# Performance work log

Hardware: AMD Instinct MI355X
Metric: run time of the kernel (lower is better)

The kernel has to match this reference:

```python
import jax, jax.numpy as jnp
import numpy as np
from jax import lax

OUT_SIZE = 224  # original input spatial size (output_size of anomaly map)
NUM_NEIGHBORS = 9
SIGMA = 4.0
KSIZE = 2 * int(4.0 * SIGMA + 0.5) + 1  # 33, kornia-style kernel size


def avg_pool3(x):
    # AvgPool2d(3, 1, 1), count_include_pad=True -> sum over 3x3 window / 9
    s = lax.reduce_window(x, 0.0, lax.add, (1, 1, 3, 3), (1, 1, 1, 1),
                          [(0, 0), (0, 0), (1, 1), (1, 1)])
    return s / 9.0


def euclidean_dist(x, y):
    # x: [..., N, E], y: [..., M, E] -> [..., N, M]
    x_norm = jnp.sum(x * x, axis=-1, keepdims=True)
    y_norm = jnp.sum(y * y, axis=-1, keepdims=True)
    res = x_norm - 2.0 * jnp.matmul(x, jnp.swapaxes(y, -2, -1)) + jnp.swapaxes(y_norm, -2, -1)
    return jnp.sqrt(jnp.clip(res, 0.0))


def gaussian_blur(x):
    # x: [B,1,H,W]; separable Gaussian, reflect padding (kornia GaussianBlur2d default)
    r = KSIZE // 2
    t = jnp.arange(KSIZE, dtype=x.dtype) - r
    k = jnp.exp(-(t * t) / (2.0 * SIGMA * SIGMA))
    k = k / jnp.sum(k)
    xp = jnp.pad(x, ((0, 0), (0, 0), (r, r), (r, r)), mode='reflect')
    kh = k.reshape(1, 1, KSIZE, 1)
    kw = k.reshape(1, 1, 1, KSIZE)
    y = lax.conv_general_dilated(xp, kh, (1, 1), 'VALID',
                                 dimension_numbers=('NCHW', 'OIHW', 'NCHW'))
    return lax.conv_general_dilated(y, kw, (1, 1), 'VALID',
                                    dimension_numbers=('NCHW', 'OIHW', 'NCHW'))


def compute_anomaly_score(patch_scores, locations, embedding, memory_bank):
    # patch_scores/locations: [B, P]; embedding: [B*P, E]; memory_bank: [M, E]
    batch, num_patches = patch_scores.shape
    bidx = jnp.arange(batch)
    max_patches = jnp.argmax(patch_scores, axis=1)                       # [B]
    max_feats = embedding.reshape(batch, num_patches, -1)[bidx, max_patches]  # [B,E]
    score = patch_scores[bidx, max_patches]                              # [B]
    nn_index = locations[bidx, max_patches]                              # [B]
    nn_sample = memory_bank[nn_index]                                    # [B,E]
    n_nb = min(NUM_NEIGHBORS, memory_bank.shape[0])
    d_bank = euclidean_dist(nn_sample, memory_bank)                      # [B,M]
    _, support = lax.top_k(-d_bank, n_nb)                                # [B,k] smallest
    sup_feats = memory_bank[support]                                     # [B,k,E]
    d = euclidean_dist(max_feats[:, None, :], sup_feats)[:, 0, :]        # [B,k]
    weights = (1.0 - jax.nn.softmax(d, axis=1))[:, 0]                    # [B]
    return weights * score


def setup_inputs() -> dict:
    key = jax.random.key(0)
    k1, k2, k3 = jax.random.split(key, 3)
    feat2 = jax.random.normal(k1, (8, 512, 28, 28), dtype=jnp.float32)
    feat3 = jax.random.normal(k2, (8, 1024, 14, 14), dtype=jnp.float32)
    memory_bank = jax.random.normal(k3, (20000, 1536), dtype=jnp.float32)
    return {'feat2': feat2, 'feat3': feat3, 'memory_bank': memory_bank}


def reference(feat2, feat3, memory_bank):
    # feature pooling (AvgPool2d(3,1,1) on each backbone layer)
    f2 = avg_pool3(feat2)
    f3 = avg_pool3(feat3)
    batch, _, height, width = f2.shape
    # generate_embedding: bilinear upsample deeper layer, concat along channels
    f3u = jax.image.resize(f3, (batch, f3.shape[1], height, width), method='bilinear')
    emb = jnp.concatenate([f2, f3u], axis=1)                 # [B,1536,28,28]
    emb_dim = emb.shape[1]
    embedding = emb.transpose(0, 2, 3, 1).reshape(-1, emb_dim)  # [B*784, 1536]
    # nearest_neighbors with n_neighbors=1
    dist = euclidean_dist(embedding, memory_bank)            # [N, M]
    patch_scores = jnp.min(dist, axis=1)
    locations = jnp.argmin(dist, axis=1)
    patch_scores = patch_scores.reshape(batch, -1)
    locations = locations.reshape(batch, -1)
    pred_score = compute_anomaly_score(patch_scores, locations, embedding, memory_bank)
    # anomaly map: bilinear upsample patch scores to input size + gaussian blur
    score_map = patch_scores.reshape(batch, 1, width, height)
    amap = jax.image.resize(score_map, (batch, 1, OUT_SIZE, OUT_SIZE), method='bilinear')
    anomaly_map = gaussian_blur(amap)
    return anomaly_map, pred_score
```

## Files before the change

### kernel.cpp

```cpp
#include <hip/hip_runtime.h>
#include <math.h>

#define NB 8
#define C2 512
#define C3 1024
#define H2 28
#define W2 28
#define H3 14
#define W3 14
#define EDIM 1536
#define PPB (H2*W2)
#define NPATCH (NB*PPB)
#define MPAD 6400
#define MBANK 20000
#define NBPAD 20096
#define NBG (NBPAD/16)
#define OUTW 224
#define NNB 9
#define KS 33
#define KR 16
#define NMT 25
#define NNTB 157
#define CHUNKS 8
#define CH (MBANK/CHUNKS)
#define MPB 64
#define NSLAB 24
#define GRPB (NSLAB*1024)

#define SXQ 63.5f
#define SYQ (127.0f/6.0f)

typedef __attribute__((ext_vector_type(4))) int   i32x4;

#define LEXLT(va,ia,vb,ib) ((va) < (vb) || ((va)==(vb) && (ia)<(ib)))
#define CSWAP(va,ia,vb,ib) { if (LEXLT(va,ia,vb,ib)) { float _tv=(vb); int _ti=(ib); (vb)=(va); (ib)=(ia); (va)=_tv; (ia)=_ti; } }

#define BAR() asm volatile("s_barrier" ::: "memory")

__device__ __forceinline__ signed char q8(float x, float s) {
  int v = (int)rintf(x * s);
  v = v > 127 ? 127 : (v < -127 ? -127 : v);
  return (signed char)v;
}
__device__ __forceinline__ size_t pk_addr(int row, int c) {
  return ((size_t)((row >> 4)*NSLAB + (c >> 6)) << 10)
       + (((c >> 4) & 3) << 8) + ((row & 15) << 4) + (c & 15);
}


__global__ __launch_bounds__(256) void pool2_kernel(const float* __restrict__ in,
    float* __restrict__ emb32, signed char* __restrict__ embp) {
  int bid = blockIdx.x;
  int cg = bid & 7; int h = (bid >> 3) % H2; int b = bid / (8*H2);
  int t = threadIdx.x;
  __shared__ float s3[3][64][29];
  for (int li = t; li < 3*64*28; li += 256) {
    int w = li % 28; int c = (li/28) & 63; int dh = li/(28*64);
    int hh = h + dh - 1;
    float v = 0.f;
    if (hh >= 0 && hh < H2) v = in[((size_t)(b*C2) + cg*64 + c)*784 + hh*28 + w];
    s3[dh][c][w] = v;
  }
  __syncthreads();
  for (int o = t; o < 64*28; o += 256) {
    int c = o & 63, w = o >> 6;
    float s = 0.f;
    #pragma unroll
    for (int dh = 0; dh < 3; ++dh) {
      s += s3[dh][c][w];
      if (w > 0)  s += s3[dh][c][w-1];
      if (w < 27) s += s3[dh][c][w+1];
    }
    s *= (1.f/9.f);
    int row = b*PPB + h*28 + w;
    int cc = cg*64 + c;
    emb32[(size_t)row*EDIM + cc] = s;
    embp[pk_addr(row, cc)] = q8(s, SXQ);
  }
}

__global__ void pool3_kernel(const float* __restrict__ in, float* __restrict__ f3p) {
  int id = blockIdx.x*blockDim.x + threadIdx.x;
  if (id >= NB*C3*H3*W3) return;
  int w = id % W3, h = (id / W3) % H3, c = (id / (H3*W3)) % C3, b = id / (C3*H3*W3);
  const float* src = in + (size_t)(b*C3 + c)*H3*W3;
  float s = 0.f;
  #pragma unroll
  for (int dh=-1; dh<=1; ++dh) {
    int hh = h+dh; if (hh<0||hh>=H3) continue;
    #pragma unroll
    for (int dw=-1; dw<=1; ++dw) {
      int ww = w+dw; if (ww<0||ww>=W3) continue;
      s += src[hh*W3+ww];
    }
  }
  f3p[(size_t)id] = s * (1.f/9.f);
}

__global__ __launch_bounds__(256) void up3_kernel(const float* __restrict__ f3p,
    float* __restrict__ emb32, signed char* __restrict__ embp) {
  int bid = blockIdx.x;
  int cg = bid & 15; int i = (bid >> 4) % H2; int b = bid / (16*H2);
  int t = threadIdx.x;
  float sy = i*0.5f - 0.25f; sy = fminf(fmaxf(sy,0.f),(float)(H3-1));
  int y0 = (int)sy; int y1 = min(y0+1,H3-1); float fy = sy - (float)y0;
  __shared__ float r2[2][64][15];
  for (int li = t; li < 2*64*14; li += 256) {
    int w = li % 14; int c = (li/14) & 63; int yy = li/(14*64);
    int ysrc = yy ? y1 : y0;
    r2[yy][c][w] = f3p[((size_t)(b*C3) + cg*64 + c)*196 + ysrc*14 + w];
  }
  __syncthreads();
  for (int o = t; o < 64*28; o += 256) {
    int c = o & 63, j = o >> 6;
    float sx = j*0.5f - 0.25f; sx = fminf(fmaxf(sx,0.f),(float)(W3-1));
    int x0 = (int)sx; int x1 = min(x0+1,W3-1); float fx = sx - (float)x0;
    float v = (1.f-fy)*((1.f-fx)*r2[0][c][x0] + fx*r2[0][c][x1])
            +      fy *((1.f-fx)*r2[1][c][x0] + fx*r2[1][c][x1]);
    int row = b*PPB + i*28 + j;
    int cc = C2 + cg*64 + c;
    emb32[(size_t)row*EDIM + cc] = v;
    embp[pk_addr(row, cc)] = q8(v, SXQ);
  }
}


__global__ void bank_yn_kernel(const float* __restrict__ bank, float* __restrict__ yn) {
  int w = (blockIdx.x*blockDim.x + threadIdx.x) >> 6;
  int lane = threadIdx.x & 63;
  if (w >= MBANK) return;
  const float4* p = reinterpret_cast<const float4*>(bank + (size_t)w*EDIM);
  float acc = 0.f;
  #pragma unroll
  for (int k = 0; k < EDIM/4/64; ++k) {
    float4 v = p[lane + k*64];
    acc = fmaf(v.x,v.x,acc); acc = fmaf(v.y,v.y,acc);
    acc = fmaf(v.z,v.z,acc); acc = fmaf(v.w,v.w,acc);
  }
  #pragma unroll
  for (int s = 32; s; s >>= 1) acc += __shfl_xor(acc, s);
  if (lane == 0) yn[w] = acc;
}

__global__ __launch_bounds__(256) void bank_pack_kernel(const float* __restrict__ bank,
                                                        signed char* __restrict__ bankp) {
  int grp = blockIdx.x;
  int t = threadIdx.x;
  #pragma unroll
  for (int q = 0; q < 6; ++q) {
    int chunk = t + 256*q;
    int p = chunk >> 6, l = chunk & 63;
    int h = l & 15, gg = l >> 4;
    int row = grp*16 + h;
    int o16[4] = {0,0,0,0};
    if (row < MBANK) {
      const float* src = bank + (size_t)row*EDIM + p*64 + gg*16;
      signed char* oc = (signed char*)o16;
      #pragma unroll
      for (int e = 0; e < 16; ++e) oc[e] = q8(src[e], SYQ);
    }
    *reinterpret_cast<int4*>(bankp + (size_t)grp*GRPB + (size_t)chunk*16) =
        make_int4(o16[0], o16[1], o16[2], o16[3]);
  }
}


__global__ __launch_bounds__(512, 4) void dist_min_i8(
    const signed char* __restrict__ Apk, const signed char* __restrict__ Bpk,
    const float* __restrict__ yn, float* __restrict__ outq, int* __restrict__ outi)
{
  __shared__ __align__(16) unsigned char LDSC[4096];
  const int t = threadIdx.x;
  const int lane = t & 63, wid = t >> 6;
  const int wr = wid >> 1, wc = wid & 1;

  const int nwg = NMT*NNTB;
  int orig = blockIdx.x;
  int xcd = orig & 7, loc = orig >> 3;
  int qq = nwg >> 3, rm = nwg & 7;
  int wg = (xcd < rm ? xcd*(qq+1) : rm*(qq+1) + (xcd-rm)*qq) + loc;
  const int mt = wg / NNTB, nt = wg % NNTB;
  const int m0 = mt*256, n0 = nt*128;

  const signed char* ap[4];
  const signed char* bp[4];
  #pragma unroll
  for (int i = 0; i < 4; ++i) {
    int m16 = (m0 >> 4) + wr*4 + i;
    ap[i] = Apk + (size_t)m16*GRPB + lane*16;
  }
  #pragma unroll
  for (int j = 0; j < 4; ++j) {
    int n16 = (n0 >> 4) + wc*4 + j;
    bp[j] = Bpk + (size_t)n16*GRPB + lane*16;
  }

  i32x4 acc[4][4];
  #pragma unroll
  for (int i = 0; i < 4; ++i)
    #pragma unroll
    for (int j = 0; j < 4; ++j) acc[i][j] = (i32x4){0,0,0,0};

  #pragma unroll 2
  for (int p = 0; p < NSLAB; ++p) {
    i32x4 af[4], bfv[4];
    #pragma unroll
    for (int j = 0; j < 4; ++j)
      bfv[j] = *(const i32x4*)(bp[j] + (size_t)p*1024);
    #pragma unroll
    for (int i = 0; i < 4; ++i)
      af[i] = *(const i32x4*)(ap[i] + (size_t)p*1024);
    __builtin_amdgcn_s_setprio(1);
    #pragma unroll
    for (int i = 0; i < 4; ++i)
      #pragma unroll
      for (int j = 0; j < 4; ++j)
        acc[i][j] = __builtin_amdgcn_mfma_i32_16x16x64_i8(af[i], bfv[j], acc[i][j], 0, 0, 0);
    __builtin_amdgcn_s_setprio(0);
    BAR();
  }

  const float NEG2INV = -2.0f * (2.0f/127.0f) * (6.0f/127.0f);
  const int h = lane & 15, g = lane >> 4;
  float ynv[4];
  #pragma unroll
  for (int j = 0; j < 4; ++j) {
    int col = n0 + wc*64 + j*16 + h;
    ynv[j] = col < MBANK ? yn[col] : INFINITY;
  }
  float* smin = (float*)LDSC;
  int* sidx = (int*)(LDSC + 2048);
  #pragma unroll
  for (int i = 0; i < 4; ++i) {
    #pragma unroll
    for (int r = 0; r < 4; ++r) {
      float v = INFINITY; int ix = 0x7fffffff;
      #pragma unroll
      for (int j = 0; j < 4; ++j) {
        float q = fmaf(NEG2INV, (float)acc[i][j][r], ynv[j]);
        int col = n0 + wc*64 + j*16 + h;
        if (q < v || (q == v && col < ix)) { v = q; ix = col; }
      }
      #pragma unroll
      for (int m = 1; m < 16; m <<= 1) {
        float ov = __shfl_xor(v, m);
        int   oi = __shfl_xor(ix, m);
        if (ov < v || (ov == v && oi < ix)) { v = ov; ix = oi; }
      }
      if (h == 0) {
        int rl = wr*64 + i*16 + g*4 + r;
        smin[rl*2 + wc] = v;
        sidx[rl*2 + wc] = ix;
      }
    }
  }
  __syncthreads();
  if (t < 256) {
    float v0 = smin[t*2], v1 = smin[t*2+1];
    int   i0 = sidx[t*2], i1 = sidx[t*2+1];
    float v; int ix;
    if (LEXLT(v1, i1, v0, i0)) { v = v1; ix = i1; } else { v = v0; ix = i0; }
    int row = m0 + t;
    if (row < NPATCH) {
      outq[(size_t)nt*NPATCH + row] = v;
      outi[(size_t)nt*NPATCH + row] = ix;
    }
  }
}


__global__ __launch_bounds__(256) void minrescore_kernel(
    const float* __restrict__ outq, const int* __restrict__ outi,
    const float* __restrict__ emb32, const float* __restrict__ bank,
    const float* __restrict__ yn, int* __restrict__ loc, float* __restrict__ ps) {
  int w = (blockIdx.x*blockDim.x + threadIdx.x) >> 6;
  int lane = threadIdx.x & 63;
  if (w >= NPATCH) return;
  float bv = INFINITY; int bi = 0x7fffffff;
  for (int s = lane; s < NNTB; s += 64) {
    float v = outq[(size_t)s*NPATCH + w];
    int  ix = outi[(size_t)s*NPATCH + w];
    if (LEXLT(v, ix, bv, bi)) { bv = v; bi = ix; }
  }
  #pragma unroll
  for (int m = 32; m; m >>= 1) {
    float ov = __shfl_xor(bv, m);
    int   oi = __shfl_xor(bi, m);
    if (LEXLT(ov, oi, bv, bi)) { bv = ov; bi = oi; }
  }
  int j = bi;
  if (lane == 0) loc[w] = j;
  const float4* x = reinterpret_cast<const float4*>(emb32 + (size_t)w*EDIM);
  const float4* y = reinterpret_cast<const float4*>(bank + (size_t)j*EDIM);
  float accd = 0.f, accx = 0.f;
  #pragma unroll
  for (int k = 0; k < EDIM/4/64; ++k) {
    float4 a = x[lane + k*64], b = y[lane + k*64];
    accd = fmaf(a.x,b.x,accd); accd = fmaf(a.y,b.y,accd);
    accd = fmaf(a.z,b.z,accd); accd = fmaf(a.w,b.w,accd);
    accx = fmaf(a.x,a.x,accx); accx = fmaf(a.y,a.y,accx);
    accx = fmaf(a.z,a.z,accx); accx = fmaf(a.w,a.w,accx);
  }
  #pragma unroll
  for (int s = 32; s; s >>= 1) { accd += __shfl_xor(accd, s); accx += __shfl_xor(accx, s); }
  if (lane == 0) ps[w] = sqrtf(fmaxf(accx - 2.f*accd + yn[j], 0.f));
}


__global__ void argmax_kernel(const float* __restrict__ ps, const int* __restrict__ loc,
                              float* __restrict__ bscore, int* __restrict__ brow, int* __restrict__ bnn) {
  __shared__ float sv[256]; __shared__ int si[256];
  int b = blockIdx.x, t = threadIdx.x;
  float bv = -INFINITY; int bi = 0x7fffffff;
  for (int p = t; p < PPB; p += 256) {
    float v = ps[b*PPB + p];
    if (v > bv || (v == bv && p < bi)) { bv = v; bi = p; }
  }
  sv[t] = bv; si[t] = bi; __syncthreads();
  for (int s = 128; s; s >>= 1) {
    if (t < s) {
      if (sv[t+s] > sv[t] || (sv[t+s] == sv[t] && si[t+s] < si[t])) { sv[t] = sv[t+s]; si[t] = si[t+s]; }
    }
    __syncthreads();
  }
  if (t == 0) {
    bscore[b] = sv[0];
    brow[b]   = b*PPB + si[0];
    bnn[b]    = loc[b*PPB + si[0]];
  }
}

__global__ __launch_bounds__(256) void dbank_kernel(
    const float* __restrict__ bank, const float* __restrict__ yn,
    const int* __restrict__ bnn, float* __restrict__ dbank)
{
  __shared__ float xs[8][EDIM];
  int t = threadIdx.x;
  for (int idx = t*4; idx < 8*EDIM; idx += 256*4) {
    int b = idx / EDIM, k = idx % EDIM;
    float4 v = *reinterpret_cast<const float4*>(bank + (size_t)bnn[b]*EDIM + k);
    *reinterpret_cast<float4*>(&xs[b][k]) = v;
  }
  __syncthreads();
  int lane = t & 63, w = t >> 6;
  for (int u = 0; u < MPB/4; ++u) {
    int m = blockIdx.x*MPB + u*4 + w;
    if (m < MBANK) {
      const float4* yp = reinterpret_cast<const float4*>(bank + (size_t)m*EDIM);
      float acc[8] = {0.f,0.f,0.f,0.f,0.f,0.f,0.f,0.f};
      for (int k4 = lane; k4 < EDIM/4; k4 += 64) {
        float4 y = yp[k4];
        int k = k4*4;
        #pragma unroll
        for (int b = 0; b < 8; ++b) {
          acc[b] = fmaf(y.x, xs[b][k+0], acc[b]);
          acc[b] = fmaf(y.y, xs[b][k+1], acc[b]);
          acc[b] = fmaf(y.z, xs[b][k+2], acc[b]);
          acc[b] = fmaf(y.w, xs[b][k+3], acc[b]);
        }
      }
      #pragma unroll
      for (int b = 0; b < 8; ++b) {
        float a = acc[b];
        #pragma unroll
        for (int s = 32; s; s >>= 1) a += __shfl_xor(a, s);
        acc[b] = a;
      }
      if (lane == 0) {
        #pragma unroll
        for (int b = 0; b < 8; ++b) {
          int nn = bnn[b];
          float d2 = yn[nn] - 2.f*acc[b] + yn[m];
          dbank[(size_t)b*MBANK + m] = sqrtf(fmaxf(d2, 0.f));
        }
      }
    }
  }
}


__global__ __launch_bounds__(256) void top9_stage1(const float* __restrict__ dbank,
                                                   float* __restrict__ cv, int* __restrict__ ci) {
  int b = blockIdx.x / CHUNKS, ch = blockIdx.x % CHUNKS;
  const float* db = dbank + (size_t)b*MBANK + ch*CH;
  int t = threadIdx.x;

  float v0=INFINITY,v1=INFINITY,v2=INFINITY,v3=INFINITY,v4=INFINITY,
        v5=INFINITY,v6=INFINITY,v7=INFINITY,v8=INFINITY;
  int i0=0x7fffffff,i1=0x7fffffff,i2=0x7fffffff,i3=0x7fffffff,i4=0x7fffffff,
      i5=0x7fffffff,i6=0x7fffffff,i7=0x7fffffff,i8=0x7fffffff;

  for (int s = 0; s < (CH+255)/256; ++s) {
    int m = t + s*256;
    if (m < CH) {
      float nv = db[m]; int ni = ch*CH + m;
      if (LEXLT(nv,ni,v8,i8)) {
        v8 = nv; i8 = ni;
        CSWAP(v8,i8,v7,i7); CSWAP(v7,i7,v6,i6); CSWAP(v6,i6,v5,i5); CSWAP(v5,i5,v4,i4);
        CSWAP(v4,i4,v3,i3); CSWAP(v3,i3,v2,i2); CSWAP(v2,i2,v1,i1); CSWAP(v1,i1,v0,i0);
      }
    }
  }

  __shared__ float sv[256*9];
  __shared__ int   si[256*9];
  __shared__ float rv[256]; __shared__ int ri[256]; __shared__ int rp[256];
  sv[t*9+0]=v0; sv[t*9+1]=v1; sv[t*9+2]=v2; sv[t*9+3]=v3; sv[t*9+4]=v4;
  sv[t*9+5]=v5; sv[t*9+6]=v6; sv[t*9+7]=v7; sv[t*9+8]=v8;
  si[t*9+0]=i0; si[t*9+1]=i1; si[t*9+2]=i2; si[t*9+3]=i3; si[t*9+4]=i4;
  si[t*9+5]=i5; si[t*9+6]=i6; si[t*9+7]=i7; si[t*9+8]=i8;
  __syncthreads();

  for (int r = 0; r < NNB; ++r) {
    float bv = INFINITY; int bix = 0x7fffffff; int bp = -1;
    #pragma unroll
    for (int u = 0; u < 9; ++u) {
      float v = sv[t*9+u]; int ix = si[t*9+u];
      if (LEXLT(v,ix,bv,bix)) { bv = v; bix = ix; bp = t*9+u; }
    }
    rv[t] = bv; ri[t] = bix; rp[t] = bp; __syncthreads();
    for (int s = 128; s; s >>= 1) {
      if (t < s) {
        if (LEXLT(rv[t+s],ri[t+s],rv[t],ri[t])) { rv[t]=rv[t+s]; ri[t]=ri[t+s]; rp[t]=rp[t+s]; }
      }
      __syncthreads();
    }
    if (t == 0) {
      cv[blockIdx.x*NNB + r] = rv[0];
      ci[blockIdx.x*NNB + r] = ri[0];
      sv[rp[0]] = INFINITY; si[rp[0]] = 0x7fffffff;
    }
    __syncthreads();
  }
}


__global__ __launch_bounds__(128) void finalize_kernel(
    const float* __restrict__ cv, const int* __restrict__ ci,
    const float* __restrict__ emb32, const float* __restrict__ bank,
    const float* __restrict__ yn, const int* __restrict__ brow,
    const float* __restrict__ bscore, float* __restrict__ out) {
  __shared__ float sv[128]; __shared__ int si[128];
  __shared__ float wv[128]; __shared__ int wi[128]; __shared__ int wp[128];
  __shared__ int supp[NNB]; __shared__ float ds[NNB];
  int b = blockIdx.x, t = threadIdx.x;
  if (t < CHUNKS*NNB) { sv[t] = cv[b*CHUNKS*NNB + t]; si[t] = ci[b*CHUNKS*NNB + t]; }
  else { sv[t] = INFINITY; si[t] = 0x7fffffff; }
  __syncthreads();
  for (int r = 0; r < NNB; ++r) {
    wv[t] = sv[t]; wi[t] = si[t]; wp[t] = t; __syncthreads();
    for (int s = 64; s; s >>= 1) {
      if (t < s) {
        if (LEXLT(wv[t+s],wi[t+s],wv[t],wi[t])) { wv[t]=wv[t+s]; wi[t]=wi[t+s]; wp[t]=wp[t+s]; }
      }
      __syncthreads();
    }
    if (t == 0) {
      supp[r] = wi[0];
      sv[wp[0]] = INFINITY; si[wp[0]] = 0x7fffffff;
    }
    __syncthreads();
  }
  int lane = t & 63, w = t >> 6;
  int row = brow[b];
  const float* x = emb32 + (size_t)row*EDIM;
  for (int j = w; j < NNB; j += 2) {
    const float* y = bank + (size_t)supp[j]*EDIM;
    float accd = 0.f, accx = 0.f;
    for (int k = lane; k < EDIM; k += 64) {
      float a = x[k];
      accd = fmaf(a, y[k], accd);
      accx = fmaf(a, a, accx);
    }
    #pragma unroll
    for (int s = 32; s; s >>= 1) { accd += __shfl_xor(accd, s); accx += __shfl_xor(accx, s); }
    if (lane == 0) ds[j] = sqrtf(fmaxf(accx - 2.f*accd + yn[supp[j]], 0.f));
  }
  __syncthreads();
  if (t == 0) {
    float mx = -INFINITY;
    #pragma unroll
    for (int j = 0; j < NNB; ++j) mx = fmaxf(mx, ds[j]);
    float s = 0.f;
    #pragma unroll
    for (int j = 0; j < NNB; ++j) s += expf(ds[j] - mx);
    float wgt = 1.f - expf(ds[0] - mx) / s;
    out[b] = wgt * bscore[b];
  }
}


__device__ __forceinline__ int refl224(int x) {
  if (x < 0) return -x;
  if (x > OUTW-1) return 2*(OUTW-1) - x;
  return x;
}

__global__ __launch_bounds__(256) void upblurh_kernel(const float* __restrict__ ps,
                                                      float* __restrict__ tmp) {
  int b = blockIdx.x / OUTW, i = blockIdx.x % OUTW;
  int t = threadIdx.x;
  __shared__ float l[W2];
  __shared__ float graw[KS];
  if (t < KS) {
    float x = (float)t - (float)KR;
    graw[t] = expf(-(x*x) / (2.f*4.f*4.f));
  }
  float sy = ((float)i + 0.5f)*0.125f - 0.5f; sy = fminf(fmaxf(sy,0.f),(float)(H2-1));
  int y0 = (int)sy; int y1 = min(y0+1,H2-1); float fy = sy - (float)y0;
  if (t < W2) {
    const float* p = ps + b*PPB;
    l[t] = (1.f-fy)*p[y0*W2+t] + fy*p[y1*W2+t];
  }
  __syncthreads();
  if (t >= OUTW) return;
  float gsum = 0.f;
  #pragma unroll
  for (int u = 0; u < KS; ++u) gsum += graw[u];
  float winv = 1.f / gsum;
  float s = 0.f;
  #pragma unroll
  for (int v = 0; v < KS; ++v) {
    int jj = refl224(t - KR + v);
    float sx = ((float)jj + 0.5f)*0.125f - 0.5f; sx = fminf(fmaxf(sx,0.f),(float)(W2-1));
    int x0 = (int)sx; int x1 = min(x0+1,W2-1); float fx = sx - (float)x0;
    s = fmaf(graw[v]*winv, (1.f-fx)*l[x0] + fx*l[x1], s);
  }
  tmp[((size_t)b*OUTW + i)*OUTW + t] = s;
}

__global__ __launch_bounds__(256) void blurv_kernel(const float* __restrict__ in,
                                                    float* __restrict__ out) {
  __shared__ float graw[KS];
  int t = threadIdx.x;
  if (t < KS) {
    float x = (float)t - (float)KR;
    graw[t] = expf(-(x*x) / (2.f*4.f*4.f));
  }
  __syncthreads();
  int id = blockIdx.x*blockDim.x + t;
  if (id >= NB*OUTW*OUTW) return;
  float gsum = 0.f;
  #pragma unroll
  for (int u = 0; u < KS; ++u) gsum += graw[u];
  float winv = 1.f / gsum;
  int j = id % OUTW, i = (id/OUTW) % OUTW, b = id/(OUTW*OUTW);
  float s = 0.f;
  #pragma unroll
  for (int u = 0; u < KS; ++u) {
    int ii = refl224(i - KR + u);
    s = fmaf(graw[u]*winv, in[((size_t)b*OUTW + ii)*OUTW + j], s);
  }
  out[id] = s;
}


extern "C" void kernel_launch(void* const* d_in, const int* in_sizes, int n_in,
                              void* d_out, int out_size, void* d_ws, size_t ws_size,
                              hipStream_t stream) {
  const float* feat2 = (const float*)d_in[0];
  const float* feat3 = (const float*)d_in[1];
  const float* bank  = (const float*)d_in[2];
  float* out = (float*)d_out;

  char* base = (char*)d_ws;
  size_t off = 0;
  auto alloc = [&](size_t nbytes) -> char* {
    char* p = base + off;
    off += ((nbytes + 255) & ~(size_t)255);
    return p;
  };
  float*       emb32 = (float*)      alloc((size_t)NPATCH*EDIM*4);
  signed char* embp  = (signed char*)alloc((size_t)(MPAD/16)*GRPB);
  signed char* bankp = (signed char*)alloc((size_t)NBG*GRPB);
  float* f3p    = (float*)alloc((size_t)NB*C3*H3*W3*4);
  float* yn     = (float*)alloc(MBANK*4);
  float* outq   = (float*)alloc((size_t)NNTB*NPATCH*4);
  int*   outi   = (int*)  alloc((size_t)NNTB*NPATCH*4);
  float* ps     = (float*)alloc(NPATCH*4);
  int*   loc    = (int*)  alloc(NPATCH*4);
  float* bscore = (float*)alloc(NB*4);
  int*   brow   = (int*)  alloc(NB*4);
  int*   bnn    = (int*)  alloc(NB*4);
  float* dbank  = (float*)alloc((size_t)NB*MBANK*4);
  float* cv     = (float*)alloc(NB*CHUNKS*NNB*4);
  int*   ci     = (int*)  alloc(NB*CHUNKS*NNB*4);
  float* tmp    = (float*)alloc((size_t)NB*OUTW*OUTW*4);

  pool2_kernel<<<NB*H2*8, 256, 0, stream>>>(feat2, emb32, embp);
  {
    int n = NB*C3*H3*W3;
    pool3_kernel<<<(n+255)/256, 256, 0, stream>>>(feat3, f3p);
  }
  up3_kernel<<<NB*H2*16, 256, 0, stream>>>(f3p, emb32, embp);
  bank_yn_kernel<<<(MBANK*64)/256, 256, 0, stream>>>(bank, yn);
  bank_pack_kernel<<<NBG, 256, 0, stream>>>(bank, bankp);

  dist_min_i8<<<NMT*NNTB, 512, 0, stream>>>(embp, bankp, yn, outq, outi);
  minrescore_kernel<<<(NPATCH*64)/256, 256, 0, stream>>>(outq, outi, emb32, bank, yn, loc, ps);

  argmax_kernel<<<NB, 256, 0, stream>>>(ps, loc, bscore, brow, bnn);
  dbank_kernel<<<(MBANK+MPB-1)/MPB, 256, 0, stream>>>(bank, yn, bnn, dbank);
  top9_stage1<<<NB*CHUNKS, 256, 0, stream>>>(dbank, cv, ci);
  finalize_kernel<<<NB, 128, 0, stream>>>(cv, ci, emb32, bank, yn, brow, bscore,
                                          out + NB*OUTW*OUTW);

  {
    upblurh_kernel<<<NB*OUTW, 256, 0, stream>>>(ps, tmp);
    int n = NB*OUTW*OUTW;
    blurv_kernel<<<(n+255)/256, 256, 0, stream>>>(tmp, out);
  }
}
```

Measured before the change: 526.7 us.

## Stage A tiles through LDS with async loads; fuse bank norm into pack

The int8 distance GEMM now loads its A operand (embedding tiles) cooperatively into a double-buffered LDS region using global_load_lds, prefetching the next slab during MFMA work. Before, each wave loaded its own A fragments straight from global memory, so A was fetched redundantly across waves. Separately, the bank squared-norm computation is folded into the bank packing kernel using LDS atomics, which removes one extra pass over the 120MB bank. The LDS footprint grows from 4KB to 32KB per block, which may limit occupancy at launch bounds (512,4). The added vmcnt waits also serialize each iteration on the B loads as well.

Result: faster. 492.8 us (-6.4%).

```diff
diff --git a/kernel.cpp b/kernel.cpp
--- a/kernel.cpp
+++ b/kernel.cpp
@@ -36,7 +36,13 @@
 #define CSWAP(va,ia,vb,ib) { if (LEXLT(va,ia,vb,ib)) { float _tv=(vb); int _ti=(ib); (vb)=(va); (ib)=(ia); (va)=_tv; (ia)=_ti; } }
 
 #define BAR() asm volatile("s_barrier" ::: "memory")
-
+#define WAITV0() asm volatile("s_waitcnt vmcnt(0)" ::: "memory")
+
+__device__ __forceinline__ void gload16(const void* g, void* l) {
+  __builtin_amdgcn_global_load_lds(
+      (const __attribute__((address_space(1))) unsigned int*)g,
+      (__attribute__((address_space(3))) unsigned int*)l, 16, 0, 0);
+}
 __device__ __forceinline__ signed char q8(float x, float s) {
   int v = (int)rintf(x * s);
   v = v > 127 ? 127 : (v < -127 ? -127 : v);
@@ -125,27 +131,14 @@
 }
 
 
-__global__ void bank_yn_kernel(const float* __restrict__ bank, float* __restrict__ yn) {
-  int w = (blockIdx.x*blockDim.x + threadIdx.x) >> 6;
-  int lane = threadIdx.x & 63;
-  if (w >= MBANK) return;
-  const float4* p = reinterpret_cast<const float4*>(bank + (size_t)w*EDIM);
-  float acc = 0.f;
-  #pragma unroll
-  for (int k = 0; k < EDIM/4/64; ++k) {
-    float4 v = p[lane + k*64];
-    acc = fmaf(v.x,v.x,acc); acc = fmaf(v.y,v.y,acc);
-    acc = fmaf(v.z,v.z,acc); acc = fmaf(v.w,v.w,acc);
-  }
-  #pragma unroll
-  for (int s = 32; s; s >>= 1) acc += __shfl_xor(acc, s);
-  if (lane == 0) yn[w] = acc;
-}
-
 __global__ __launch_bounds__(256) void bank_pack_kernel(const float* __restrict__ bank,
-                                                        signed char* __restrict__ bankp) {
+                                                        signed char* __restrict__ bankp,
+                                                        float* __restrict__ yn) {
+  __shared__ float rn[16];
   int grp = blockIdx.x;
   int t = threadIdx.x;
+  if (t < 16) rn[t] = 0.f;
+  __syncthreads();
   #pragma unroll
   for (int q = 0; q < 6; ++q) {
     int chunk = t + 256*q;
@@ -156,12 +149,16 @@
     if (row < MBANK) {
       const float* src = bank + (size_t)row*EDIM + p*64 + gg*16;
       signed char* oc = (signed char*)o16;
+      float ls = 0.f;
       #pragma unroll
-      for (int e = 0; e < 16; ++e) oc[e] = q8(src[e], SYQ);
+      for (int e = 0; e < 16; ++e) { float v = src[e]; ls = fmaf(v, v, ls); oc[e] = q8(v, SYQ); }
+      atomicAdd(&rn[h], ls);
     }
     *reinterpret_cast<int4*>(bankp + (size_t)grp*GRPB + (size_t)chunk*16) =
         make_int4(o16[0], o16[1], o16[2], o16[3]);
   }
+  __syncthreads();
+  if (t < 16 && grp*16 + t < MBANK) yn[grp*16 + t] = rn[t];
 }
 
 
@@ -169,7 +166,7 @@
     const signed char* __restrict__ Apk, const signed char* __restrict__ Bpk,
     const float* __restrict__ yn, float* __restrict__ outq, int* __restrict__ outi)
 {
-  __shared__ __align__(16) unsigned char LDSC[4096];
+  __shared__ __align__(16) unsigned char LDSC[32768];
   const int t = threadIdx.x;
   const int lane = t & 63, wid = t >> 6;
   const int wr = wid >> 1, wc = wid & 1;
@@ -182,18 +179,18 @@
   const int mt = wg / NNTB, nt = wg % NNTB;
   const int m0 = mt*256, n0 = nt*128;
 
-  const signed char* ap[4];
+  const int gA = (m0 >> 4) + wid*2;
+  const signed char* aSrc0 = Apk + (size_t)gA*GRPB + lane*16;
+  const signed char* aSrc1 = Apk + (size_t)(gA+1)*GRPB + lane*16;
+  const unsigned aDstOff = (unsigned)(wid*2048);
+
   const signed char* bp[4];
-  #pragma unroll
-  for (int i = 0; i < 4; ++i) {
-    int m16 = (m0 >> 4) + wr*4 + i;
-    ap[i] = Apk + (size_t)m16*GRPB + lane*16;
-  }
   #pragma unroll
   for (int j = 0; j < 4; ++j) {
     int n16 = (n0 >> 4) + wc*4 + j;
     bp[j] = Bpk + (size_t)n16*GRPB + lane*16;
   }
+  const unsigned aRd = (unsigned)((wr*4)*1024 + lane*16);
 
   i32x4 acc[4][4];
   #pragma unroll
@@ -201,15 +198,26 @@
     #pragma unroll
     for (int j = 0; j < 4; ++j) acc[i][j] = (i32x4){0,0,0,0};
 
-  #pragma unroll 2
+  gload16(aSrc0, (char*)LDSC + aDstOff);
+  gload16(aSrc1, (char*)LDSC + aDstOff + 1024);
+  WAITV0();
+  BAR();
+
   for (int p = 0; p < NSLAB; ++p) {
-    i32x4 af[4], bfv[4];
+    const unsigned sb = (unsigned)(p & 1)*16384u;
+    i32x4 bfv[4];
     #pragma unroll
     for (int j = 0; j < 4; ++j)
       bfv[j] = *(const i32x4*)(bp[j] + (size_t)p*1024);
+    if (p < NSLAB-1) {
+      const unsigned sw = (unsigned)((p+1) & 1)*16384u;
+      gload16(aSrc0 + (size_t)(p+1)*1024, (char*)LDSC + sw + aDstOff);
+      gload16(aSrc1 + (size_t)(p+1)*1024, (char*)LDSC + sw + aDstOff + 1024);
+    }
+    i32x4 af[4];
     #pragma unroll
     for (int i = 0; i < 4; ++i)
-      af[i] = *(const i32x4*)(ap[i] + (size_t)p*1024);
+      af[i] = *(const i32x4*)(LDSC + sb + aRd + i*1024);
     __builtin_amdgcn_s_setprio(1);
     #pragma unroll
     for (int i = 0; i < 4; ++i)
@@ -217,6 +225,7 @@
       for (int j = 0; j < 4; ++j)
         acc[i][j] = __builtin_amdgcn_mfma_i32_16x16x64_i8(af[i], bfv[j], acc[i][j], 0, 0, 0);
     __builtin_amdgcn_s_setprio(0);
+    WAITV0();
     BAR();
   }
 
@@ -593,8 +602,7 @@
     pool3_kernel<<<(n+255)/256, 256, 0, stream>>>(feat3, f3p);
   }
   up3_kernel<<<NB*H2*16, 256, 0, stream>>>(f3p, emb32, embp);
-  bank_yn_kernel<<<(MBANK*64)/256, 256, 0, stream>>>(bank, yn);
-  bank_pack_kernel<<<NBG, 256, 0, stream>>>(bank, bankp);
+  bank_pack_kernel<<<NBG, 256, 0, stream>>>(bank, bankp, yn);
 
   dist_min_i8<<<NMT*NNTB, 512, 0, stream>>>(embp, bankp, yn, outq, outi);
   minrescore_kernel<<<(NPATCH*64)/256, 256, 0, stream>>>(outq, outi, emb32, bank, yn, loc, ps);
```
